# Kernel tuning notes

Measured on AMD Instinct MI355X. Metric: run time of the kernel, lower is better.

## Reference

```python
import jax, jax.numpy as jnp
import numpy as np

ALPHA = 0.9
T = 809          # doc_len_limit hard-coded in fofe_tricontext_encoder
M = 16           # opt['max_len'] (cand_len_limit)
BN_EPS = 1e-5


def _cand_indices(T, M):
    # Enumeration order matches get_sample_index: outer over start s, inner over span.
    s_list, e_list = [], []
    for s in range(T):
        for span in range(min(M, T - s)):
            s_list.append(s)
            e_list.append(s + span)
    return np.asarray(s_list, np.int32), np.asarray(e_list, np.int32)

_S_IDX, _E_IDX = _cand_indices(T, M)          # [N_CANDS] = [12824]
_SPAN = (_E_IDX - _S_IDX).astype(np.int64)
# FOFE decay coefficient alpha^(e-s+1) for subtracting the prefix before the span
_COEF = (ALPHA ** (_SPAN + 1)).astype(np.float32)
# Lower-triangular FOFE prefix operator: A[t,k] = alpha^(t-k) for k<=t
_DIFF = np.subtract.outer(np.arange(T), np.arange(T))
_AFWD = np.where(_DIFF >= 0, ALPHA ** np.maximum(_DIFF, 0), 0.0).astype(np.float32)


def _bn(x, g, b, m, v):
    return (x - m) * jax.lax.rsqrt(v + BN_EPS) * g + b


def _forward(doc_emb, query_emb, W1, g1, b1, m1, v1, W2, g2, b2, m2, v2, W3):
    B, Tt, Dd = doc_emb.shape
    A = jnp.asarray(_AFWD)
    # forward FOFE prefixes F[t] = sum_{k<=t} alpha^(t-k) x[k]; inverse FOFE suffixes
    F = jnp.einsum('tk,bkd->btd', A, doc_emb)          # [B,T,Dd]
    R = jnp.einsum('tk,bkd->btd', A.T, doc_emb)        # [B,T,Dd]
    Fp = jnp.concatenate([jnp.zeros((B, 1, Dd), F.dtype), F], axis=1)   # Fp[:,s]=F[s-1]
    Rp = jnp.concatenate([R, jnp.zeros((B, 1, Dd), R.dtype)], axis=1)   # Rp[:,e+1]
    s_idx = jnp.asarray(_S_IDX)
    e_idx = jnp.asarray(_E_IDX)
    coef = jnp.asarray(_COEF)
    lctx = Fp[:, s_idx]                                 # left context excl cand
    cand = F[:, e_idx] - coef[None, :, None] * Fp[:, s_idx]  # FOFE of span [s,e]
    rctx = Rp[:, e_idx + 1]                             # right context excl cand
    doc_fofe = jnp.concatenate([lctx, cand, rctx], axis=-1)  # [B,N,3*Dd]
    # query FOFE (fofe_linear): z = sum_t alpha^(Lq-1-t) q[t]
    Lq = query_emb.shape[1]
    w = (ALPHA ** jnp.arange(Lq - 1, -1, -1, dtype=jnp.float32))
    qf = jnp.einsum('t,btd->bd', w, query_emb)          # [B,E]
    N = doc_fofe.shape[1]
    qf_b = jnp.broadcast_to(qf[:, None, :], (B, N, qf.shape[-1]))
    dq = jnp.concatenate([doc_fofe, qf_b], axis=-1)     # [B,N,3*Dd+E]
    x = dq.reshape(B * N, -1)
    h = jax.nn.relu(_bn(x @ W1.T, g1, b1, m1, v1))      # 1x1 conv == GEMM
    h = jax.nn.relu(_bn(h @ W2.T, g2, b2, m2, v2))
    out = (h @ W3.T).reshape(B, N, 2)                   # 2 class scores per candidate
    return out


def setup_inputs() -> dict:
    key = jax.random.key(0)
    ks = jax.random.split(key, 13)
    B, Lq, Dd, E = 4, 30, 304, 300
    Cin, H4, H2 = 3 * Dd + E, 1024, 512
    return {
        'doc_emb': jax.random.normal(ks[0], (B, T, Dd), jnp.float32),
        'query_emb': jax.random.normal(ks[1], (B, Lq, E), jnp.float32),
        'W1': jax.random.normal(ks[2], (H4, Cin), jnp.float32) / np.sqrt(Cin),
        'g1': jax.random.normal(ks[3], (H4,), jnp.float32),
        'b1': jax.random.normal(ks[4], (H4,), jnp.float32),
        'm1': jax.random.normal(ks[5], (H4,), jnp.float32),
        'v1': jax.random.uniform(ks[6], (H4,), jnp.float32),
        'W2': jax.random.normal(ks[7], (H2, H4), jnp.float32) / np.sqrt(H4),
        'g2': jax.random.normal(ks[8], (H2,), jnp.float32),
        'b2': jax.random.normal(ks[9], (H2,), jnp.float32),
        'm2': jax.random.normal(ks[10], (H2,), jnp.float32),
        'v2': jax.random.uniform(ks[11], (H2,), jnp.float32),
        'W3': jax.random.normal(ks[12], (2, H2), jnp.float32) / np.sqrt(H2),
    }


def reference(doc_emb, query_emb, W1, g1, b1, m1, v1, W2, g2, b2, m2, v2, W3):
    return _forward(doc_emb, query_emb, W1, g1, b1, m1, v1, W2, g2, b2, m2, v2, W3)
```

## Files before the change

### kernel.cpp

```cpp
#include <hip/hip_runtime.h>
#include <string.h>

#define T_LEN   809
#define DD      304
#define EE      300
#define LQ      30
#define NCAND   12824
#define NPAD    12928
#define CIN     1212
#define H1      1024
#define H2      512
#define BATCH   4
#define MROWS_F (BATCH * NPAD)
#define KS      320
#define TPAD    3328

#define MP_SCAN0   0
#define MP_W1      416
#define MP_W2      4256
#define MP_BIAS2   6304
#define MP_BASE    6306
#define MP_TOTAL   7330

__device__ __constant__ float c_coef[16] = {
  0.9f, 0.81f, 0.729f, 0.6561f, 0.59049f, 0.531441f, 0.4782969f, 0.43046721f,
  0.387420489f, 0.3486784401f, 0.31381059609f, 0.282429536481f,
  0.2541865828329f, 0.22876792454961f, 0.205891132094649f, 0.1853020188851841f
};

__device__ __forceinline__ unsigned short f2bf(float f) {
  unsigned int u = __float_as_uint(f);
  u += 0x7fffu + ((u >> 16) & 1u);
  return (unsigned short)(u >> 16);
}
__device__ __forceinline__ float bf2f(unsigned int h) {
  return __uint_as_float(h << 16);
}

typedef const __attribute__((address_space(1))) unsigned int GU32;
typedef __attribute__((address_space(3))) unsigned int LU32;
__device__ __forceinline__ void async16(const unsigned short* g, unsigned short* l) {
  __builtin_amdgcn_global_load_lds((GU32*)g, (LU32*)l, 16, 0, 0);
}

__global__ __launch_bounds__(256) void k_prep(const float* __restrict__ doc,
                                              const float* __restrict__ qe,
                                              const float* __restrict__ W1,
                                              const float* __restrict__ g1,
                                              const float* __restrict__ b1,
                                              const float* __restrict__ m1,
                                              const float* __restrict__ v1,
                                              const float* __restrict__ W2,
                                              const float* __restrict__ g2,
                                              const float* __restrict__ b2,
                                              const float* __restrict__ m2,
                                              const float* __restrict__ v2,
                                              unsigned short* __restrict__ Fz,
                                              unsigned short* __restrict__ Rz,
                                              unsigned short* __restrict__ Wlc,
                                              unsigned short* __restrict__ Wr,
                                              unsigned short* __restrict__ W2b,
                                              float* __restrict__ bias2,
                                              float* __restrict__ baseW)
{
  __shared__ float qs[EE];
  const int vb  = blockIdx.x;
  const int tid = threadIdx.x;

  if (vb < MP_W1) {
    const int dchunk = vb & 1;
    const int rest   = vb >> 1;
    const int tchunk = rest % 26;
    const int b      = (rest / 26) & 3;
    const int dir    = rest / 104;
    const int d  = dchunk * 256 + tid;
    const int t0 = tchunk * 32;
    if (dir == 0) {
      if (tchunk == 0 && d < KS) Fz[((size_t)b * 810) * KS + d] = 0;
      if (d >= DD) return;
      const float* db = doc + (size_t)b * T_LEN * DD + d;
      int start = t0 - 96; if (start < 0) start = 0;
      int end = t0 + 31; if (end > T_LEN - 1) end = T_LEN - 1;
      float s = 0.f;
      for (int t = start; t <= end; ++t) {
        s = fmaf(0.9f, s, db[(size_t)t * DD]);
        if (t >= t0) Fz[((size_t)b * 810 + 1 + t) * KS + d] = f2bf(s);
      }
    } else {
      if (tchunk == 0 && d < KS) Rz[((size_t)b * 810 + 809) * KS + d] = 0;
      if (d >= DD) return;
      const float* db = doc + (size_t)b * T_LEN * DD + d;
      int t1 = t0 + 31; if (t1 > T_LEN - 1) t1 = T_LEN - 1;
      int start = t1 + 96; if (start > T_LEN - 1) start = T_LEN - 1;
      float s = 0.f;
      for (int t = start; t >= t0; --t) {
        s = fmaf(0.9f, s, db[(size_t)t * DD]);
        if (t <= t1) Rz[((size_t)b * 810 + t) * KS + d] = f2bf(s);
      }
    }
  } else if (vb < MP_W2) {
    const int e = (vb - MP_W1) * 256 + tid;
    const int j = e / KS;
    const int k = e - j * KS;
    int jj, koff; unsigned short* dst; size_t idx;
    if (j < 1024)      { jj = j;        koff = k;       dst = Wlc; idx = (size_t)j * KS + k; }
    else if (j < 2048) { jj = j - 1024; koff = 304 + k; dst = Wlc; idx = (size_t)j * KS + k; }
    else               { jj = j - 2048; koff = 608 + k; dst = Wr;  idx = (size_t)(j - 2048) * KS + k; }
    float w = 0.f;
    if (k < 304) w = W1[(size_t)jj * CIN + koff] * g1[jj] * rsqrtf(v1[jj] + 1e-5f);
    dst[idx] = f2bf(w);
  } else if (vb < MP_BIAS2) {
    const int e = (vb - MP_W2) * 256 + tid;
    const int j = e >> 10;
    const int k = e & 1023;
    const float w = W2[(size_t)j * H1 + k] * g2[j] * rsqrtf(v2[j] + 1e-5f);
    W2b[(size_t)j * H1 + k] = f2bf(w);
  } else if (vb < MP_BASE) {
    const int i = (vb - MP_BIAS2) * 256 + tid;
    if (i < H2) {
      const float s = g2[i] * rsqrtf(v2[i] + 1e-5f);
      bias2[i] = b2[i] - m2[i] * s;
    }
  } else {
    const int flat = vb - MP_BASE;
    const int b  = flat >> 8;
    const int jg = flat & 255;
    const float* q = qe + (size_t)b * LQ * EE;
    for (int k = tid; k < EE; k += 256) {
      float s = 0.f;
      for (int t = 0; t < LQ; ++t) s = fmaf(s, 0.9f, q[(size_t)t * EE + k]);
      qs[k] = s;
    }
    __syncthreads();
    const int wv   = tid >> 6;
    const int lane = tid & 63;
    const int j = jg * 4 + wv;
    const float* w = W1 + (size_t)j * CIN + 912;
    float acc = 0.f;
    for (int k = lane; k < EE; k += 64) acc = fmaf(qs[k], w[k], acc);
    #pragma unroll
    for (int off = 32; off; off >>= 1) acc += __shfl_down(acc, off);
    if (lane == 0) {
      const float sc = g1[j] * rsqrtf(v1[j] + 1e-5f);
      baseW[(size_t)b * 2048 + j]        = b1[j] - m1[j] * sc + acc * sc;
      baseW[(size_t)b * 2048 + 1024 + j] = 0.f;
    }
  }
}

typedef __attribute__((ext_vector_type(8))) short frag8;
typedef __attribute__((ext_vector_type(4))) float f32x4;

#define GEMM_KLOOP(A_, B_, K_)                                                   \
  __shared__ __align__(16) unsigned short As[128 * 32];                          \
  __shared__ __align__(16) unsigned short Bs[128 * 32];                          \
  const int tid  = threadIdx.x;                                                  \
  const int lane = tid & 63;                                                     \
  const int wv   = tid >> 6;                                                     \
  const int wm   = wv & 1, wn = wv >> 1;                                         \
  const int lr = lane >> 2;                                                      \
  const int lc = lane & 3;                                                       \
  const int sc = lc ^ ((lr >> 1) & 3);                                           \
  const unsigned short* gA = A_ + ((size_t)bm * 128 + wv * 32 + lr) * K_ + sc * 8; \
  const unsigned short* gB = B_ + ((size_t)bn * 128 + wv * 32 + lr) * K_ + sc * 8; \
  const size_t row16 = (size_t)16 * K_;                                          \
  unsigned short* lA0 = &As[wv * 1024];                                          \
  unsigned short* lB0 = &Bs[wv * 1024];                                          \
  f32x4 acc[4][4];                                                               \
  _Pragma("unroll")                                                              \
  for (int i = 0; i < 4; ++i)                                                    \
    _Pragma("unroll")                                                            \
    for (int j = 0; j < 4; ++j) acc[i][j] = (f32x4){0.f, 0.f, 0.f, 0.f};         \
  const int arow = lane & 15;                                                    \
  const int pg   = (lane >> 4) ^ ((arow >> 1) & 3);                              \
  const int aoff = (wm * 64 + arow) * 32 + pg * 8;                               \
  const int boff = (wn * 64 + arow) * 32 + pg * 8;                               \
  for (int kc = 0; kc < K_; kc += 32) {                                          \
    __syncthreads();                                                             \
    async16(gA + kc,         lA0);                                               \
    async16(gA + kc + row16, lA0 + 512);                                         \
    async16(gB + kc,         lB0);                                               \
    async16(gB + kc + row16, lB0 + 512);                                         \
    __syncthreads();                                                             \
    frag8 a[4], b[4];                                                            \
    _Pragma("unroll")                                                            \
    for (int i = 0; i < 4; ++i) a[i] = *(const frag8*)&As[aoff + i * 512];       \
    _Pragma("unroll")                                                            \
    for (int i = 0; i < 4; ++i) b[i] = *(const frag8*)&Bs[boff + i * 512];       \
    _Pragma("unroll")                                                            \
    for (int i = 0; i < 4; ++i)                                                  \
      _Pragma("unroll")                                                          \
      for (int j = 0; j < 4; ++j)                                                \
        acc[i][j] = __builtin_amdgcn_mfma_f32_16x16x32_bf16(a[i], b[j], acc[i][j], 0, 0, 0); \
  }

__global__ __launch_bounds__(256, 4) void k_ugemm(const unsigned short* __restrict__ Fz,
                                                  const unsigned short* __restrict__ Wlc,
                                                  const unsigned short* __restrict__ Rz,
                                                  const unsigned short* __restrict__ Wr,
                                                  const float* __restrict__ baseW,
                                                  unsigned short* __restrict__ UF,
                                                  unsigned short* __restrict__ UR)
{
  int bx = blockIdx.x;
  const int isUF = (bx < 416);
  const unsigned short *Ap, *Bp; unsigned short* Cp; int bn, bm, Nout;
  if (isUF) { Ap = Fz; Bp = Wlc; Cp = UF; bn = bx & 15; bm = bx >> 4; Nout = 2048; }
  else { bx -= 416; Ap = Rz; Bp = Wr; Cp = UR; bn = bx & 7; bm = bx >> 3; Nout = 1024; }
  GEMM_KLOOP(Ap, Bp, KS)
  const int crow0 = bm * 128 + wm * 64 + ((lane >> 4) << 2);
  const int ccol0 = bn * 128 + wn * 64 + arow;
  #pragma unroll
  for (int i = 0; i < 4; ++i)
    #pragma unroll
    for (int j = 0; j < 4; ++j) {
      const int col = ccol0 + j * 16;
      #pragma unroll
      for (int r = 0; r < 4; ++r) {
        const int row = crow0 + i * 16 + r;
        float v = acc[i][j][r];
        if (isUF) {
          int bb = row / 810; if (bb > 3) bb = 3;
          v += baseW[(size_t)bb * 2048 + col];
        }
        Cp[(size_t)row * Nout + col] = f2bf(v);
      }
    }
}

__global__ __launch_bounds__(512) void k_combine(const unsigned short* __restrict__ UF,
                                                 const unsigned short* __restrict__ UR,
                                                 unsigned short* __restrict__ h1)
{
  __shared__ float s_ul[1024];
  __shared__ float s_ucs[1024];
  const int flat = (blockIdx.x & 7) * 405 + (blockIdx.x >> 3);
  if (flat >= BATCH * T_LEN) return;
  const int b = flat / T_LEN;
  const int s = flat - b * T_LEN;
  const int oct = threadIdx.x >> 6;
  const int t = threadIdx.x & 63;
  const size_t rs = (size_t)b * 810 + s;
  const int e0 = t * 16;

  {
    const unsigned int u = *(const unsigned int*)(UF + rs * 2048 + threadIdx.x * 2);
    const unsigned int c = *(const unsigned int*)(UF + rs * 2048 + 1024 + threadIdx.x * 2);
    s_ul[threadIdx.x * 2]      = bf2f(u & 0xffff);
    s_ul[threadIdx.x * 2 + 1]  = bf2f(u >> 16);
    s_ucs[threadIdx.x * 2]     = bf2f(c & 0xffff);
    s_ucs[threadIdx.x * 2 + 1] = bf2f(c >> 16);
  }
  __syncthreads();

  float ul[16], ucs[16];
  #pragma unroll
  for (int k = 0; k < 4; ++k) {
    const float4 a = *(const float4*)&s_ul[e0 + k * 4];
    const float4 c = *(const float4*)&s_ucs[e0 + k * 4];
    ul[4*k] = a.x; ul[4*k+1] = a.y; ul[4*k+2] = a.z; ul[4*k+3] = a.w;
    ucs[4*k] = c.x; ucs[4*k+1] = c.y; ucs[4*k+2] = c.z; ucs[4*k+3] = c.w;
  }

  const int nspan = min(16, T_LEN - s);
  int r0;
  if (s < 794) r0 = s * 16;
  else { const int d = s - 794; r0 = 12704 + 15 * d - (d * (d - 1)) / 2; }

  #pragma unroll
  for (int sp = 0; sp < 16; sp += 8) {
    const int row = sp + oct;
    if (row < nspan) {
      const size_t re = rs + row + 1;
      const uint4 e0v = *(const uint4*)(UF + re * 2048 + 1024 + e0);
      const uint4 e1v = *(const uint4*)(UF + re * 2048 + 1024 + e0 + 8);
      const uint4 r0v = *(const uint4*)(UR + re * 1024 + e0);
      const uint4 r1v = *(const uint4*)(UR + re * 1024 + e0 + 8);
      const float c = c_coef[row];
      const unsigned int* pe0 = (const unsigned int*)&e0v;
      const unsigned int* pe1 = (const unsigned int*)&e1v;
      const unsigned int* pr0 = (const unsigned int*)&r0v;
      const unsigned int* pr1 = (const unsigned int*)&r1v;
      unsigned int o[8];
      #pragma unroll
      for (int i = 0; i < 4; ++i) {
        float xlo = ul[2*i]   + bf2f(pe0[i] & 0xffff) - c * ucs[2*i]   + bf2f(pr0[i] & 0xffff);
        float xhi = ul[2*i+1] + bf2f(pe0[i] >> 16)    - c * ucs[2*i+1] + bf2f(pr0[i] >> 16);
        xlo = xlo > 0.f ? xlo : 0.f;
        xhi = xhi > 0.f ? xhi : 0.f;
        o[i] = (unsigned int)f2bf(xlo) | ((unsigned int)f2bf(xhi) << 16);
        float ylo = ul[8+2*i]   + bf2f(pe1[i] & 0xffff) - c * ucs[8+2*i]   + bf2f(pr1[i] & 0xffff);
        float yhi = ul[8+2*i+1] + bf2f(pe1[i] >> 16)    - c * ucs[8+2*i+1] + bf2f(pr1[i] >> 16);
        ylo = ylo > 0.f ? ylo : 0.f;
        yhi = yhi > 0.f ? yhi : 0.f;
        o[4 + i] = (unsigned int)f2bf(ylo) | ((unsigned int)f2bf(yhi) << 16);
      }
      unsigned short* dst = h1 + ((size_t)b * NPAD + r0 + row) * H1 + e0;
      *(uint4*)dst = *(const uint4*)&o[0];
      *(uint4*)(dst + 8) = *(const uint4*)&o[4];
    }
  }
}

__global__ __launch_bounds__(256, 4) void k_gemm2p(const unsigned short* __restrict__ A,
                                                   const unsigned short* __restrict__ W2b,
                                                   const float* __restrict__ bias,
                                                   const float* __restrict__ W3,
                                                   float* __restrict__ P)
{
  const int global = blockIdx.x * 202 + blockIdx.y;
  const int bm = global >> 2;
  const int bn = global & 3;
  __shared__ float red[2][4][4][4][2];
  GEMM_KLOOP(A, W2b, H1)

  const int ccol0 = bn * 128 + wn * 64 + arow;
  float bj[4], w0[4], w1[4];
  #pragma unroll
  for (int j = 0; j < 4; ++j) {
    const int col = ccol0 + j * 16;
    bj[j] = bias[col];
    w0[j] = W3[col];
    w1[j] = W3[H2 + col];
  }
  float p0[4][4], p1[4][4];
  #pragma unroll
  for (int i = 0; i < 4; ++i)
    #pragma unroll
    for (int r = 0; r < 4; ++r) {
      float q0 = 0.f, q1 = 0.f;
      #pragma unroll
      for (int j = 0; j < 4; ++j) {
        float v = acc[i][j][r] + bj[j];
        v = v > 0.f ? v : 0.f;
        q0 = fmaf(v, w0[j], q0);
        q1 = fmaf(v, w1[j], q1);
      }
      #pragma unroll
      for (int m = 1; m < 16; m <<= 1) {
        q0 += __shfl_xor(q0, m);
        q1 += __shfl_xor(q1, m);
      }
      p0[i][r] = q0; p1[i][r] = q1;
    }

  const int grp = lane >> 4;
  if (wn == 1 && arow == 0) {
    #pragma unroll
    for (int i = 0; i < 4; ++i)
      #pragma unroll
      for (int r = 0; r < 4; ++r) {
        red[wm][i][r][grp][0] = p0[i][r];
        red[wm][i][r][grp][1] = p1[i][r];
      }
  }
  __syncthreads();
  if (wn == 0 && arow == 0) {
    #pragma unroll
    for (int i = 0; i < 4; ++i)
      #pragma unroll
      for (int r = 0; r < 4; ++r) {
        const size_t row = (size_t)bm * 128 + wm * 64 + grp * 4 + i * 16 + r;
        P[row * 8 + bn * 2 + 0] = p0[i][r] + red[wm][i][r][grp][0];
        P[row * 8 + bn * 2 + 1] = p1[i][r] + red[wm][i][r][grp][1];
      }
  }
}

__global__ __launch_bounds__(256) void k_fin(const float* __restrict__ P, float* __restrict__ out)
{
  const int row = blockIdx.x * 256 + threadIdx.x;
  if (row >= MROWS_F) return;
  const int b = row / NPAD;
  const int rr = row - b * NPAD;
  if (rr >= NCAND) return;
  const float4 pa = ((const float4*)P)[row * 2];
  const float4 pb = ((const float4*)P)[row * 2 + 1];
  float* o = out + ((size_t)b * NCAND + rr) * 2;
  o[0] = pa.x + pa.z + pb.x + pb.z;
  o[1] = pa.y + pa.w + pb.y + pb.w;
}

extern "C" void kernel_launch(void* const* d_in, const int* in_sizes, int n_in,
                              void* d_out, int out_size, void* d_ws, size_t ws_size,
                              hipStream_t stream)
{
  const float* doc = (const float*)d_in[0];
  const float* qe  = (const float*)d_in[1];
  const float* W1  = (const float*)d_in[2];
  const float* g1  = (const float*)d_in[3];
  const float* b1  = (const float*)d_in[4];
  const float* m1  = (const float*)d_in[5];
  const float* v1  = (const float*)d_in[6];
  const float* W2  = (const float*)d_in[7];
  const float* g2  = (const float*)d_in[8];
  const float* b2  = (const float*)d_in[9];
  const float* m2  = (const float*)d_in[10];
  const float* v2  = (const float*)d_in[11];
  const float* W3  = (const float*)d_in[12];
  float* out = (float*)d_out;

  char* ws = (char*)d_ws;
  size_t off = 0;
  auto alloc = [&](size_t bytes) -> void* {
    void* p = ws + off;
    off = (off + bytes + 255) & ~(size_t)255;
    return p;
  };
  unsigned short* Fz    = (unsigned short*)alloc((size_t)TPAD * KS * 2);
  unsigned short* Rz    = (unsigned short*)alloc((size_t)TPAD * KS * 2);
  unsigned short* Wlc   = (unsigned short*)alloc((size_t)2048 * KS * 2);
  unsigned short* Wr    = (unsigned short*)alloc((size_t)1024 * KS * 2);
  unsigned short* W2b   = (unsigned short*)alloc((size_t)H2 * H1 * 2);
  float*          bias2 = (float*)alloc((size_t)H2 * 4);
  float*          baseW = (float*)alloc((size_t)BATCH * 2048 * 4);
  unsigned short* UF    = (unsigned short*)alloc((size_t)TPAD * 2048 * 2);
  unsigned short* UR    = (unsigned short*)alloc((size_t)TPAD * 1024 * 2);
  unsigned short* h1    = (unsigned short*)alloc((size_t)MROWS_F * H1 * 2);
  float*          P     = (float*)alloc((size_t)MROWS_F * 8 * 4);
  (void)ws_size;

  k_prep<<<dim3(MP_TOTAL), 256, 0, stream>>>(doc, qe, W1, g1, b1, m1, v1,
                                             W2, g2, b2, m2, v2,
                                             Fz, Rz, Wlc, Wr, W2b, bias2, baseW);
  k_ugemm<<<dim3(416 + 208), 256, 0, stream>>>(Fz, Wlc, Rz, Wr, baseW, UF, UR);
  k_combine<<<dim3(8 * 405), 512, 0, stream>>>(UF, UR, h1);
  k_gemm2p<<<dim3(8, 202), 256, 0, stream>>>(h1, W2b, bias2, W3, P);
  k_fin<<<dim3((MROWS_F + 255) / 256), 256, 0, stream>>>(P, out);
}
```

Before: 230.5 us.

## Replace second GEMM with 256x256-tile, 8-wave double-buffered async-LDS pipelined kernel

Rewrites the H1→H2 GEMM with a fused ReLU/W3 projection epilogue. It now uses 256x256 output tiles on 512-thread blocks with four-quadrant phases, double-buffered async global-to-LDS staging, explicit waitcnt/barrier scheduling, setprio around MFMA bursts and an XCD-aware block remap. Larger tiles cut A/B re-reads and halve the partial-sum buffer, so the final reduction kernel only adds two partials. The cost is heavy LDS use (128 KB), fewer blocks in flight, and hand-tuned synchronisation that is fragile.

```diff
diff --git a/kernel.cpp b/kernel.cpp
--- a/kernel.cpp
+++ b/kernel.cpp
@@ -302,69 +302,165 @@
   }
 }
 
-__global__ __launch_bounds__(256, 4) void k_gemm2p(const unsigned short* __restrict__ A,
-                                                   const unsigned short* __restrict__ W2b,
+#define NT_K   16
+#define NITER  8
+
+__global__ __launch_bounds__(512, 2) void k_gemm2x(const unsigned short* __restrict__ A,
+                                                   const unsigned short* __restrict__ B,
                                                    const float* __restrict__ bias,
                                                    const float* __restrict__ W3,
                                                    float* __restrict__ P)
 {
-  const int global = blockIdx.x * 202 + blockIdx.y;
-  const int bm = global >> 2;
-  const int bn = global & 3;
-  __shared__ float red[2][4][4][4][2];
-  GEMM_KLOOP(A, W2b, H1)
-
-  const int ccol0 = bn * 128 + wn * 64 + arow;
-  float bj[4], w0[4], w1[4];
+  __shared__ __align__(16) unsigned short L[65536];
+
+  const int orig = blockIdx.x;
+  const int xcd = orig & 7, cidx = orig >> 3;
+  const int wg = (xcd < 4 ? xcd * 51 : 204 + (xcd - 4) * 50) + cidx;
+  const int bm = wg >> 1, bn = wg & 1;
+
+  const int tid  = threadIdx.x;
+  const int w    = tid >> 6;
+  const int lane = tid & 63;
+  const int wr = w >> 2, wc = w & 3;
+  const int arow = lane & 15;
+  const int acol_sh = ((((lane >> 4) << 4) ^ ((arow & 8) << 2)) >> 1);
+
+  const int cs   = tid ^ (((tid >> 5) & 1) << 1);
+  const size_t srcOff = ((size_t)(cs >> 2) << 10) + (size_t)((cs & 3) << 3);
+  const unsigned short* Ab = A + ((size_t)bm << 18) + srcOff;
+  const unsigned short* Bb = B + ((size_t)bn << 18) + srcOff;
+  unsigned short* ldsw = &L[w * 512];
+
+  const int aBase = (wr * 64 + arow) * 32 + acol_sh;
+  const int bBase = 16384 + (wc * 32 + arow) * 32 + acol_sh;
+
+  f32x4 acc[2][2][4][2];
   #pragma unroll
-  for (int j = 0; j < 4; ++j) {
-    const int col = ccol0 + j * 16;
-    bj[j] = bias[col];
-    w0[j] = W3[col];
-    w1[j] = W3[H2 + col];
-  }
-  float p0[4][4], p1[4][4];
+  for (int qm = 0; qm < 2; ++qm)
+    #pragma unroll
+    for (int qn = 0; qn < 2; ++qn)
+      #pragma unroll
+      for (int i = 0; i < 4; ++i)
+        #pragma unroll
+        for (int j = 0; j < 2; ++j) acc[qm][qn][i][j] = (f32x4){0.f, 0.f, 0.f, 0.f};
+
+#define STAGE(buf_, isB_, half_, kt_)                                                 \
+  {                                                                                   \
+    const unsigned short* s_ = (isB_ ? Bb : Ab) + (size_t)(half_) * 131072 + (kt_) * 64; \
+    unsigned short* d_ = ldsw + (buf_) * 32768 + (isB_) * 16384 + (half_) * 8192;     \
+    async16(s_,      d_);                                                             \
+    async16(s_ + 32, d_ + 4096);                                                      \
+  }
+
+#define PHASE(q_, qm_, qn_, VMW_, ...)                                                \
+  {                                                                                   \
+    frag8 af[4][2], bf[2][2];                                                         \
+    _Pragma("unroll")                                                                 \
+    for (int ks = 0; ks < 2; ++ks) {                                                  \
+      _Pragma("unroll")                                                               \
+      for (int i = 0; i < 4; ++i)                                                     \
+        af[i][ks] = *(const frag8*)&L[(q_)*32768 + (qm_)*8192 + ks*4096 + i*512 + aBase]; \
+      _Pragma("unroll")                                                               \
+      for (int j = 0; j < 2; ++j)                                                     \
+        bf[j][ks] = *(const frag8*)&L[(q_)*32768 + (qn_)*8192 + ks*4096 + j*512 + bBase]; \
+    }                                                                                 \
+    __VA_ARGS__                                                                       \
+    __builtin_amdgcn_sched_barrier(0);                                                \
+    __builtin_amdgcn_s_barrier();                                                     \
+    asm volatile("s_waitcnt lgkmcnt(0)" ::: "memory");                                \
+    __builtin_amdgcn_sched_barrier(0);                                                \
+    __builtin_amdgcn_s_setprio(1);                                                    \
+    _Pragma("unroll")                                                                 \
+    for (int ks = 0; ks < 2; ++ks)                                                    \
+      _Pragma("unroll")                                                               \
+      for (int i = 0; i < 4; ++i)                                                     \
+        _Pragma("unroll")                                                             \
+        for (int j = 0; j < 2; ++j)                                                   \
+          acc[qm_][qn_][i][j] = __builtin_amdgcn_mfma_f32_16x16x32_bf16(              \
+              af[i][ks], bf[j][ks], acc[qm_][qn_][i][j], 0, 0, 0);                    \
+    __builtin_amdgcn_s_setprio(0);                                                    \
+    VMW_;                                                                             \
+    __builtin_amdgcn_s_barrier();                                                     \
+    __builtin_amdgcn_sched_barrier(0);                                                \
+  }
+
+#define VM_PF()                                                                       \
+  { if (pf) asm volatile("s_waitcnt vmcnt(4)" ::: "memory");                          \
+    else    asm volatile("s_waitcnt vmcnt(0)" ::: "memory"); }
+#define VM_NONE()
+
+  STAGE(0, 0, 0, 0);
+  STAGE(0, 1, 0, 0);
+  STAGE(0, 0, 1, 0);
+  STAGE(0, 1, 1, 0);
+  STAGE(1, 0, 0, 1);
+  STAGE(1, 1, 0, 1);
+  asm volatile("s_waitcnt vmcnt(4)" ::: "memory");
+  __builtin_amdgcn_s_barrier();
+  __builtin_amdgcn_sched_barrier(0);
+
+  for (int it = 0; it < NITER; ++it) {
+    const int t = it * 2;
+    const bool pf = (it < NITER - 1);
+    PHASE(0, 0, 0, VM_NONE(), STAGE(1, 0, 1, t + 1);)
+    PHASE(0, 0, 1, VM_NONE(), STAGE(1, 1, 1, t + 1);)
+    PHASE(0, 1, 0, VM_NONE(), if (pf) STAGE(0, 0, 0, t + 2);)
+    PHASE(0, 1, 1, VM_PF(),   if (pf) STAGE(0, 1, 0, t + 2);)
+    PHASE(1, 0, 0, VM_NONE(), if (pf) STAGE(0, 0, 1, t + 2);)
+    PHASE(1, 0, 1, VM_NONE(), if (pf) STAGE(0, 1, 1, t + 2);)
+    PHASE(1, 1, 0, VM_NONE(), if (pf) STAGE(1, 0, 0, t + 3);)
+    PHASE(1, 1, 1, VM_PF(),   if (pf) STAGE(1, 1, 0, t + 3);)
+  }
+
+  __syncthreads();
+  float* redf = (float*)L;
+
+  float bj[2][2], w0v[2][2], w1v[2][2];
   #pragma unroll
-  for (int i = 0; i < 4; ++i)
+  for (int qn = 0; qn < 2; ++qn)
     #pragma unroll
-    for (int r = 0; r < 4; ++r) {
-      float q0 = 0.f, q1 = 0.f;
-      #pragma unroll
-      for (int j = 0; j < 4; ++j) {
-        float v = acc[i][j][r] + bj[j];
-        v = v > 0.f ? v : 0.f;
-        q0 = fmaf(v, w0[j], q0);
-        q1 = fmaf(v, w1[j], q1);
-      }
-      #pragma unroll
-      for (int m = 1; m < 16; m <<= 1) {
-        q0 += __shfl_xor(q0, m);
-        q1 += __shfl_xor(q1, m);
-      }
-      p0[i][r] = q0; p1[i][r] = q1;
-    }
-
-  const int grp = lane >> 4;
-  if (wn == 1 && arow == 0) {
+    for (int j = 0; j < 2; ++j) {
+      const int col = bn * 256 + qn * 128 + wc * 32 + j * 16 + arow;
+      bj[qn][j]  = bias[col];
+      w0v[qn][j] = W3[col];
+      w1v[qn][j] = W3[H2 + col];
+    }
+  const int g = lane >> 4;
+  #pragma unroll
+  for (int qm = 0; qm < 2; ++qm)
     #pragma unroll
     for (int i = 0; i < 4; ++i)
       #pragma unroll
       for (int r = 0; r < 4; ++r) {
-        red[wm][i][r][grp][0] = p0[i][r];
-        red[wm][i][r][grp][1] = p1[i][r];
+        float s0 = 0.f, s1 = 0.f;
+        #pragma unroll
+        for (int qn = 0; qn < 2; ++qn)
+          #pragma unroll
+          for (int j = 0; j < 2; ++j) {
+            float v = acc[qm][qn][i][j][r] + bj[qn][j];
+            v = v > 0.f ? v : 0.f;
+            s0 = fmaf(v, w0v[qn][j], s0);
+            s1 = fmaf(v, w1v[qn][j], s1);
+          }
+        #pragma unroll
+        for (int m = 1; m < 16; m <<= 1) { s0 += __shfl_xor(s0, m); s1 += __shfl_xor(s1, m); }
+        if (arow == 0) {
+          const int rl = qm * 128 + wr * 64 + i * 16 + g * 4 + r;
+          redf[(rl * 4 + wc) * 2]     = s0;
+          redf[(rl * 4 + wc) * 2 + 1] = s1;
+        }
       }
-  }
   __syncthreads();
-  if (wn == 0 && arow == 0) {
-    #pragma unroll
-    for (int i = 0; i < 4; ++i)
-      #pragma unroll
-      for (int r = 0; r < 4; ++r) {
-        const size_t row = (size_t)bm * 128 + wm * 64 + grp * 4 + i * 16 + r;
-        P[row * 8 + bn * 2 + 0] = p0[i][r] + red[wm][i][r][grp][0];
-        P[row * 8 + bn * 2 + 1] = p1[i][r] + red[wm][i][r][grp][1];
-      }
-  }
+  {
+    const int rl = tid >> 1, s = tid & 1;
+    const float v = redf[(rl * 4 + 0) * 2 + s] + redf[(rl * 4 + 1) * 2 + s]
+                  + redf[(rl * 4 + 2) * 2 + s] + redf[(rl * 4 + 3) * 2 + s];
+    P[((size_t)(bm * 256 + rl)) * 4 + bn * 2 + s] = v;
+  }
+#undef STAGE
+#undef PHASE
+#undef VM_PF
+#undef VM_NONE
 }
 
 __global__ __launch_bounds__(256) void k_fin(const float* __restrict__ P, float* __restrict__ out)
@@ -374,11 +470,10 @@
   const int b = row / NPAD;
   const int rr = row - b * NPAD;
   if (rr >= NCAND) return;
-  const float4 pa = ((const float4*)P)[row * 2];
-  const float4 pb = ((const float4*)P)[row * 2 + 1];
+  const float4 pa = ((const float4*)P)[row];
   float* o = out + ((size_t)b * NCAND + rr) * 2;
-  o[0] = pa.x + pa.z + pb.x + pb.z;
-  o[1] = pa.y + pa.w + pb.y + pb.w;
+  o[0] = pa.x + pa.z;
+  o[1] = pa.y + pa.w;
 }
 
 extern "C" void kernel_launch(void* const* d_in, const int* in_sizes, int n_in,
@@ -417,7 +512,7 @@
   unsigned short* UF    = (unsigned short*)alloc((size_t)TPAD * 2048 * 2);
   unsigned short* UR    = (unsigned short*)alloc((size_t)TPAD * 1024 * 2);
   unsigned short* h1    = (unsigned short*)alloc((size_t)MROWS_F * H1 * 2);
-  float*          P     = (float*)alloc((size_t)MROWS_F * 8 * 4);
+  float*          P     = (float*)alloc((size_t)MROWS_F * 4 * 4);
   (void)ws_size;
 
   k_prep<<<dim3(MP_TOTAL), 256, 0, stream>>>(doc, qe, W1, g1, b1, m1, v1,
@@ -425,6 +520,6 @@
                                              Fz, Rz, Wlc, Wr, W2b, bias2, baseW);
   k_ugemm<<<dim3(416 + 208), 256, 0, stream>>>(Fz, Wlc, Rz, Wr, baseW, UF, UR);
   k_combine<<<dim3(8 * 405), 512, 0, stream>>>(UF, UR, h1);
-  k_gemm2p<<<dim3(8, 202), 256, 0, stream>>>(h1, W2b, bias2, W3, P);
+  k_gemm2x<<<dim3(404), 512, 0, stream>>>(h1, W2b, bias2, W3, P);
   k_fin<<<dim3((MROWS_F + 255) / 256), 256, 0, stream>>>(P, out);
 }
```

Measured after the change: 235.0 us. Within noise of the previous version (+1.9%).

## Fuse candidate combine into second GEMM's A-tile load via row map

Applied to the files above, without the earlier changes.

Drops the materialized h1 activation buffer. The span combine (left + end - coef*cand-start, ReLU) is now computed on the fly while the second GEMM loads its A tile, using a precomputed per-row map of start/end rows and span. A small pre-kernel pre-adds the UF end part and UR so each A element needs three loads instead of four. This avoids writing and re-reading the large B*NPAD x 1024 bf16 intermediate. In exchange the A loads become synchronous gathers with ALU work inside the k-loop, losing the async LDS copy for A and lowering the occupancy hint from 4 to 3. The extra pre-add also rounds to bf16 one more time.

```diff
diff --git a/kernel.cpp b/kernel.cpp
--- a/kernel.cpp
+++ b/kernel.cpp
@@ -14,13 +14,15 @@
 #define MROWS_F (BATCH * NPAD)
 #define KS      320
 #define TPAD    3328
+#define NROWS_U 3240
 
 #define MP_SCAN0   0
 #define MP_W1      416
 #define MP_W2      4256
 #define MP_BIAS2   6304
 #define MP_BASE    6306
-#define MP_TOTAL   7330
+#define MP_RMAP    7330
+#define MP_TOTAL   7532
 
 __device__ __constant__ float c_coef[16] = {
   0.9f, 0.81f, 0.729f, 0.6561f, 0.59049f, 0.531441f, 0.4782969f, 0.43046721f,
@@ -41,6 +43,20 @@
 typedef __attribute__((address_space(3))) unsigned int LU32;
 __device__ __forceinline__ void async16(const unsigned short* g, unsigned short* l) {
   __builtin_amdgcn_global_load_lds((GU32*)g, (LU32*)l, 16, 0, 0);
+}
+
+__device__ __forceinline__ unsigned int comb2(unsigned int ul, unsigned int uc,
+                                              unsigned int ue, float cf) {
+  float xlo = bf2f(ul & 0xffff) + bf2f(ue & 0xffff) - cf * bf2f(uc & 0xffff);
+  float xhi = bf2f(ul >> 16)    + bf2f(ue >> 16)    - cf * bf2f(uc >> 16);
+  xlo = xlo > 0.f ? xlo : 0.f;
+  xhi = xhi > 0.f ? xhi : 0.f;
+  return (unsigned int)f2bf(xlo) | ((unsigned int)f2bf(xhi) << 16);
+}
+__device__ __forceinline__ unsigned int add2(unsigned int a, unsigned int b) {
+  const float lo = bf2f(a & 0xffff) + bf2f(b & 0xffff);
+  const float hi = bf2f(a >> 16)    + bf2f(b >> 16);
+  return (unsigned int)f2bf(lo) | ((unsigned int)f2bf(hi) << 16);
 }
 
 __global__ __launch_bounds__(256) void k_prep(const float* __restrict__ doc,
@@ -61,7 +77,8 @@
                                               unsigned short* __restrict__ Wr,
                                               unsigned short* __restrict__ W2b,
                                               float* __restrict__ bias2,
-                                              float* __restrict__ baseW)
+                                              float* __restrict__ baseW,
+                                              unsigned int* __restrict__ rowmap)
 {
   __shared__ float qs[EE];
   const int vb  = blockIdx.x;
@@ -121,7 +138,7 @@
       const float s = g2[i] * rsqrtf(v2[i] + 1e-5f);
       bias2[i] = b2[i] - m2[i] * s;
     }
-  } else {
+  } else if (vb < MP_RMAP) {
     const int flat = vb - MP_BASE;
     const int b  = flat >> 8;
     const int jg = flat & 255;
@@ -145,6 +162,26 @@
       baseW[(size_t)b * 2048 + j]        = b1[j] - m1[j] * sc + acc * sc;
       baseW[(size_t)b * 2048 + 1024 + j] = 0.f;
     }
+  } else {
+    const int g = (vb - MP_RMAP) * 256 + tid;
+    const int b  = g / NPAD;
+    const int rr = g - b * NPAD;
+    unsigned int mv = 0;
+    if (rr < NCAND) {
+      int s, span;
+      if (rr < 12704) { s = rr >> 4; span = rr & 15; }
+      else {
+        const int x = rr - 12704;
+        int d = 0;
+        while (d < 14 && x >= (15 * (d + 1) - ((d + 1) * d) / 2)) ++d;
+        span = x - (15 * d - (d * (d - 1)) / 2);
+        s = 794 + d;
+      }
+      const unsigned int srow = (unsigned int)(b * 810 + s);
+      const unsigned int erow = (unsigned int)(b * 810 + s + span + 1);
+      mv = srow | (erow << 12) | ((unsigned int)span << 24);
+    }
+    rowmap[g] = mv;
   }
 }
 
@@ -228,91 +265,110 @@
     }
 }
 
-__global__ __launch_bounds__(512) void k_combine(const unsigned short* __restrict__ UF,
-                                                 const unsigned short* __restrict__ UR,
-                                                 unsigned short* __restrict__ h1)
-{
-  __shared__ float s_ul[1024];
-  __shared__ float s_ucs[1024];
-  const int flat = (blockIdx.x & 7) * 405 + (blockIdx.x >> 3);
-  if (flat >= BATCH * T_LEN) return;
-  const int b = flat / T_LEN;
-  const int s = flat - b * T_LEN;
-  const int oct = threadIdx.x >> 6;
-  const int t = threadIdx.x & 63;
-  const size_t rs = (size_t)b * 810 + s;
-  const int e0 = t * 16;
-
-  {
-    const unsigned int u = *(const unsigned int*)(UF + rs * 2048 + threadIdx.x * 2);
-    const unsigned int c = *(const unsigned int*)(UF + rs * 2048 + 1024 + threadIdx.x * 2);
-    s_ul[threadIdx.x * 2]      = bf2f(u & 0xffff);
-    s_ul[threadIdx.x * 2 + 1]  = bf2f(u >> 16);
-    s_ucs[threadIdx.x * 2]     = bf2f(c & 0xffff);
-    s_ucs[threadIdx.x * 2 + 1] = bf2f(c >> 16);
-  }
-  __syncthreads();
-
-  float ul[16], ucs[16];
-  #pragma unroll
-  for (int k = 0; k < 4; ++k) {
-    const float4 a = *(const float4*)&s_ul[e0 + k * 4];
-    const float4 c = *(const float4*)&s_ucs[e0 + k * 4];
-    ul[4*k] = a.x; ul[4*k+1] = a.y; ul[4*k+2] = a.z; ul[4*k+3] = a.w;
-    ucs[4*k] = c.x; ucs[4*k+1] = c.y; ucs[4*k+2] = c.z; ucs[4*k+3] = c.w;
-  }
-
-  const int nspan = min(16, T_LEN - s);
-  int r0;
-  if (s < 794) r0 = s * 16;
-  else { const int d = s - 794; r0 = 12704 + 15 * d - (d * (d - 1)) / 2; }
-
-  #pragma unroll
-  for (int sp = 0; sp < 16; sp += 8) {
-    const int row = sp + oct;
-    if (row < nspan) {
-      const size_t re = rs + row + 1;
-      const uint4 e0v = *(const uint4*)(UF + re * 2048 + 1024 + e0);
-      const uint4 e1v = *(const uint4*)(UF + re * 2048 + 1024 + e0 + 8);
-      const uint4 r0v = *(const uint4*)(UR + re * 1024 + e0);
-      const uint4 r1v = *(const uint4*)(UR + re * 1024 + e0 + 8);
-      const float c = c_coef[row];
-      const unsigned int* pe0 = (const unsigned int*)&e0v;
-      const unsigned int* pe1 = (const unsigned int*)&e1v;
-      const unsigned int* pr0 = (const unsigned int*)&r0v;
-      const unsigned int* pr1 = (const unsigned int*)&r1v;
-      unsigned int o[8];
-      #pragma unroll
-      for (int i = 0; i < 4; ++i) {
-        float xlo = ul[2*i]   + bf2f(pe0[i] & 0xffff) - c * ucs[2*i]   + bf2f(pr0[i] & 0xffff);
-        float xhi = ul[2*i+1] + bf2f(pe0[i] >> 16)    - c * ucs[2*i+1] + bf2f(pr0[i] >> 16);
-        xlo = xlo > 0.f ? xlo : 0.f;
-        xhi = xhi > 0.f ? xhi : 0.f;
-        o[i] = (unsigned int)f2bf(xlo) | ((unsigned int)f2bf(xhi) << 16);
-        float ylo = ul[8+2*i]   + bf2f(pe1[i] & 0xffff) - c * ucs[8+2*i]   + bf2f(pr1[i] & 0xffff);
-        float yhi = ul[8+2*i+1] + bf2f(pe1[i] >> 16)    - c * ucs[8+2*i+1] + bf2f(pr1[i] >> 16);
-        ylo = ylo > 0.f ? ylo : 0.f;
-        yhi = yhi > 0.f ? yhi : 0.f;
-        o[4 + i] = (unsigned int)f2bf(ylo) | ((unsigned int)f2bf(yhi) << 16);
-      }
-      unsigned short* dst = h1 + ((size_t)b * NPAD + r0 + row) * H1 + e0;
-      *(uint4*)dst = *(const uint4*)&o[0];
-      *(uint4*)(dst + 8) = *(const uint4*)&o[4];
-    }
-  }
-}
-
-__global__ __launch_bounds__(256, 4) void k_gemm2p(const unsigned short* __restrict__ A,
+__global__ __launch_bounds__(256) void k_ucr(const unsigned short* __restrict__ UF,
+                                             const unsigned short* __restrict__ UR,
+                                             unsigned short* __restrict__ UCR)
+{
+  const int c = blockIdx.x * 256 + threadIdx.x;
+  if (c >= NROWS_U * 128) return;
+  const int t  = c >> 7;
+  const int kk = (c & 127) * 8;
+  const uint4 a = *(const uint4*)(UF + (size_t)t * 2048 + 1024 + kk);
+  const uint4 b = *(const uint4*)(UR + (size_t)t * 1024 + kk);
+  uint4 o;
+  o.x = add2(a.x, b.x);
+  o.y = add2(a.y, b.y);
+  o.z = add2(a.z, b.z);
+  o.w = add2(a.w, b.w);
+  *(uint4*)(UCR + (size_t)t * 1024 + kk) = o;
+}
+
+__global__ __launch_bounds__(256, 3) void k_gemm2f(const unsigned short* __restrict__ UF,
+                                                   const unsigned short* __restrict__ UCR,
                                                    const unsigned short* __restrict__ W2b,
+                                                   const unsigned int* __restrict__ rowmap,
                                                    const float* __restrict__ bias,
                                                    const float* __restrict__ W3,
                                                    float* __restrict__ P)
 {
+  __shared__ __align__(16) unsigned short As[128 * 32];
+  __shared__ __align__(16) unsigned short Bs[128 * 32];
+  __shared__ float red[2][4][4][4][2];
+
   const int global = blockIdx.x * 202 + blockIdx.y;
   const int bm = global >> 2;
   const int bn = global & 3;
-  __shared__ float red[2][4][4][4][2];
-  GEMM_KLOOP(A, W2b, H1)
+  const int tid  = threadIdx.x;
+  const int lane = tid & 63;
+  const int wv   = tid >> 6;
+  const int wm   = wv & 1, wn = wv >> 1;
+  const int lr = lane >> 2;
+  const int lc = lane & 3;
+  const int sc = lc ^ ((lr >> 1) & 3);
+
+  const unsigned short* gB = W2b + ((size_t)bn * 128 + wv * 32 + lr) * H1 + sc * 8;
+  unsigned short* lB0 = &Bs[wv * 1024];
+
+  const int g0 = bm * 128 + wv * 32 + lr;
+  const unsigned int m0 = rowmap[g0];
+  const unsigned int m1 = rowmap[g0 + 16];
+  const float cf0 = c_coef[m0 >> 24];
+  const float cf1 = c_coef[m1 >> 24];
+  const unsigned short* pUL0 = UF  + (size_t)(m0 & 4095) * 2048 + sc * 8;
+  const unsigned short* pUE0 = UCR + (size_t)((m0 >> 12) & 4095) * 1024 + sc * 8;
+  const unsigned short* pUL1 = UF  + (size_t)(m1 & 4095) * 2048 + sc * 8;
+  const unsigned short* pUE1 = UCR + (size_t)((m1 >> 12) & 4095) * 1024 + sc * 8;
+  unsigned short* wA0 = &As[wv * 1024 + lane * 8];
+
+  f32x4 acc[4][4];
+  #pragma unroll
+  for (int i = 0; i < 4; ++i)
+    #pragma unroll
+    for (int j = 0; j < 4; ++j) acc[i][j] = (f32x4){0.f, 0.f, 0.f, 0.f};
+
+  const int arow = lane & 15;
+  const int pg   = (lane >> 4) ^ ((arow >> 1) & 3);
+  const int aoff = (wm * 64 + arow) * 32 + pg * 8;
+  const int boff = (wn * 64 + arow) * 32 + pg * 8;
+
+  for (int kc = 0; kc < H1; kc += 32) {
+    __syncthreads();
+    async16(gB + kc,                   lB0);
+    async16(gB + kc + (size_t)16 * H1, lB0 + 512);
+    {
+      const uint4 vul = *(const uint4*)(pUL0 + kc);
+      const uint4 vuc = *(const uint4*)(pUL0 + 1024 + kc);
+      const uint4 vue = *(const uint4*)(pUE0 + kc);
+      uint4 o;
+      o.x = comb2(vul.x, vuc.x, vue.x, cf0);
+      o.y = comb2(vul.y, vuc.y, vue.y, cf0);
+      o.z = comb2(vul.z, vuc.z, vue.z, cf0);
+      o.w = comb2(vul.w, vuc.w, vue.w, cf0);
+      *(uint4*)wA0 = o;
+    }
+    {
+      const uint4 vul = *(const uint4*)(pUL1 + kc);
+      const uint4 vuc = *(const uint4*)(pUL1 + 1024 + kc);
+      const uint4 vue = *(const uint4*)(pUE1 + kc);
+      uint4 o;
+      o.x = comb2(vul.x, vuc.x, vue.x, cf1);
+      o.y = comb2(vul.y, vuc.y, vue.y, cf1);
+      o.z = comb2(vul.z, vuc.z, vue.z, cf1);
+      o.w = comb2(vul.w, vuc.w, vue.w, cf1);
+      *(uint4*)(wA0 + 512) = o;
+    }
+    __syncthreads();
+    frag8 a[4], b[4];
+    #pragma unroll
+    for (int i = 0; i < 4; ++i) a[i] = *(const frag8*)&As[aoff + i * 512];
+    #pragma unroll
+    for (int i = 0; i < 4; ++i) b[i] = *(const frag8*)&Bs[boff + i * 512];
+    #pragma unroll
+    for (int i = 0; i < 4; ++i)
+      #pragma unroll
+      for (int j = 0; j < 4; ++j)
+        acc[i][j] = __builtin_amdgcn_mfma_f32_16x16x32_bf16(a[i], b[j], acc[i][j], 0, 0, 0);
+  }
 
   const int ccol0 = bn * 128 + wn * 64 + arow;
   float bj[4], w0[4], w1[4];
@@ -416,15 +472,16 @@
   float*          baseW = (float*)alloc((size_t)BATCH * 2048 * 4);
   unsigned short* UF    = (unsigned short*)alloc((size_t)TPAD * 2048 * 2);
   unsigned short* UR    = (unsigned short*)alloc((size_t)TPAD * 1024 * 2);
-  unsigned short* h1    = (unsigned short*)alloc((size_t)MROWS_F * H1 * 2);
+  unsigned short* UCR   = (unsigned short*)alloc((size_t)NROWS_U * 1024 * 2);
+  unsigned int*   rowmap= (unsigned int*)alloc((size_t)MROWS_F * 4);
   float*          P     = (float*)alloc((size_t)MROWS_F * 8 * 4);
   (void)ws_size;
 
   k_prep<<<dim3(MP_TOTAL), 256, 0, stream>>>(doc, qe, W1, g1, b1, m1, v1,
                                              W2, g2, b2, m2, v2,
-                                             Fz, Rz, Wlc, Wr, W2b, bias2, baseW);
+                                             Fz, Rz, Wlc, Wr, W2b, bias2, baseW, rowmap);
   k_ugemm<<<dim3(416 + 208), 256, 0, stream>>>(Fz, Wlc, Rz, Wr, baseW, UF, UR);
-  k_combine<<<dim3(8 * 405), 512, 0, stream>>>(UF, UR, h1);
-  k_gemm2p<<<dim3(8, 202), 256, 0, stream>>>(h1, W2b, bias2, W3, P);
+  k_ucr<<<dim3((NROWS_U * 128 + 255) / 256), 256, 0, stream>>>(UF, UR, UCR);
+  k_gemm2f<<<dim3(8, 202), 256, 0, stream>>>(UF, UCR, W2b, rowmap, bias2, W3, P);
   k_fin<<<dim3((MROWS_F + 255) / 256), 256, 0, stream>>>(P, out);
 }
```

New measurement: 250.6 us. 8.7% more time.
